# Performance work log

Hardware: AMD Instinct MI355X
Metric: run time of the kernel (lower is better)

Reference implementation:

```python
import jax, jax.numpy as jnp
import numpy as np

N = 4096  # rows == cols so the original's range(len(d1)) loop covers the full tensor
EPS = 1e-05


def setup_inputs() -> dict:
    key = jax.random.key(0)
    k1, k2 = jax.random.split(key)
    distribution1 = jax.random.uniform(k1, (N, N), dtype=jnp.float32)
    distribution2 = jax.random.uniform(k2, (N, N), dtype=jnp.float32)
    return {"distribution1": distribution1, "distribution2": distribution2}


def reference(distribution1, distribution2):
    d1 = jnp.squeeze(distribution1).astype(jnp.float32)
    d2 = jnp.squeeze(distribution2).astype(jnp.float32)
    # loss = sum_i [ -sum_j d1[i,j] * log(d2[i,j] + eps) ]  (fused elementwise + full reduce)
    loss = -jnp.sum(d1 * jnp.log(d2 + EPS))
    return loss.reshape(1)
```

## Files before the change

### kernel.cpp

```cpp
#include <hip/hip_runtime.h>
#include <math.h>


#define EPS 1e-5f
#define BLOCK 256
#define GRID 2048
#define STRIDE (GRID * BLOCK)

typedef float f4v __attribute__((ext_vector_type(4)));

#define LOAD2(Y, X, PB, PA)                                          \
    asm volatile("global_load_dwordx4 %0, %2, off sc0 sc1 nt\n\t"    \
                 "global_load_dwordx4 %1, %3, off sc0 sc1 nt"        \
                 : "=&v"(Y), "=&v"(X)                                \
                 : "v"(PB), "v"(PA)                                  \
                 : "memory")

#define WAITV(N)                                              \
    do {                                                      \
        asm volatile("s_waitcnt vmcnt(" #N ")" ::: "memory"); \
        __builtin_amdgcn_sched_barrier(0);                    \
    } while (0)

#define CP(X, Y)                                              \
    do {                                                      \
        acc0 = fmaf((X).x, __logf((Y).x + EPS), acc0);        \
        acc1 = fmaf((X).y, __logf((Y).y + EPS), acc1);        \
        acc2 = fmaf((X).z, __logf((Y).z + EPS), acc2);        \
        acc3 = fmaf((X).w, __logf((Y).w + EPS), acc3);        \
    } while (0)

__global__ __launch_bounds__(BLOCK) void cep_loss_kernel(
        const f4v* __restrict__ d1,
        const f4v* __restrict__ d2,
        float* __restrict__ partials) {
    const int tid = blockIdx.x * BLOCK + threadIdx.x;
    const f4v* pa = d1 + tid;
    const f4v* pb = d2 + tid;

    float acc0 = 0.0f, acc1 = 0.0f, acc2 = 0.0f, acc3 = 0.0f;

    f4v x0, x1, x2, x3, x4, x5, x6, x7;
    f4v y0, y1, y2, y3, y4, y5, y6, y7;

    LOAD2(y0, x0, pb, pa); pb += STRIDE; pa += STRIDE;
    LOAD2(y1, x1, pb, pa); pb += STRIDE; pa += STRIDE;
    LOAD2(y2, x2, pb, pa); pb += STRIDE; pa += STRIDE;
    LOAD2(y3, x3, pb, pa); pb += STRIDE; pa += STRIDE;

    WAITV(6); LOAD2(y4, x4, pb, pa); pb += STRIDE; pa += STRIDE; CP(x0, y0);
    WAITV(6); LOAD2(y5, x5, pb, pa); pb += STRIDE; pa += STRIDE; CP(x1, y1);
    WAITV(6); LOAD2(y6, x6, pb, pa); pb += STRIDE; pa += STRIDE; CP(x2, y2);
    WAITV(6); LOAD2(y7, x7, pb, pa);                             CP(x3, y3);

    WAITV(6); CP(x4, y4);
    WAITV(4); CP(x5, y5);
    WAITV(2); CP(x6, y6);
    WAITV(0); CP(x7, y7);

    float acc = (acc0 + acc1) + (acc2 + acc3);

    #pragma unroll
    for (int off = 32; off > 0; off >>= 1)
        acc += __shfl_down(acc, off, 64);

    __shared__ float wave_sums[BLOCK / 64];
    int lane = threadIdx.x & 63;
    int wid  = threadIdx.x >> 6;
    if (lane == 0) wave_sums[wid] = acc;
    __syncthreads();

    if (threadIdx.x == 0) {
        float s = wave_sums[0] + wave_sums[1] + wave_sums[2] + wave_sums[3];
        partials[blockIdx.x] = s;
    }
}

__global__ __launch_bounds__(BLOCK) void cep_final_kernel(
        const float* __restrict__ partials, float* __restrict__ out, int nparts) {
    float acc = 0.0f;
    for (int i = threadIdx.x; i < nparts; i += BLOCK)
        acc += partials[i];

    #pragma unroll
    for (int off = 32; off > 0; off >>= 1)
        acc += __shfl_down(acc, off, 64);

    __shared__ float wave_sums[BLOCK / 64];
    int lane = threadIdx.x & 63;
    int wid  = threadIdx.x >> 6;
    if (lane == 0) wave_sums[wid] = acc;
    __syncthreads();

    if (threadIdx.x == 0) {
        float s = wave_sums[0] + wave_sums[1] + wave_sums[2] + wave_sums[3];
        out[0] = -s;
    }
}

extern "C" void kernel_launch(void* const* d_in, const int* in_sizes, int n_in,
                              void* d_out, int out_size, void* d_ws, size_t ws_size,
                              hipStream_t stream) {
    const f4v* d1 = (const f4v*)d_in[0];
    const f4v* d2 = (const f4v*)d_in[1];
    float* out      = (float*)d_out;
    float* partials = (float*)d_ws;

    cep_loss_kernel<<<GRID, BLOCK, 0, stream>>>(d1, d2, partials);
    cep_final_kernel<<<1, BLOCK, 0, stream>>>(partials, out, GRID);
}
```

Baseline: 139.7 us.

## Route distribution2 loads through direct global-to-LDS async copies

```diff
diff --git a/kernel.cpp b/kernel.cpp
--- a/kernel.cpp
+++ b/kernel.cpp
@@ -9,17 +9,23 @@
 
 typedef float f4v __attribute__((ext_vector_type(4)));
 
-#define LOAD2(Y, X, PB, PA)                                          \
-    asm volatile("global_load_dwordx4 %0, %2, off sc0 sc1 nt\n\t"    \
-                 "global_load_dwordx4 %1, %3, off sc0 sc1 nt"        \
-                 : "=&v"(Y), "=&v"(X)                                \
-                 : "v"(PB), "v"(PA)                                  \
-                 : "memory")
+#define AS1 __attribute__((address_space(1)))
+#define AS3 __attribute__((address_space(3)))
+
+#define LOADX(X, PA)                                                 \
+    asm volatile("global_load_dwordx4 %0, %1, off sc0 sc1 nt"        \
+                 : "=&v"(X) : "v"(PA) : "memory")
 
 #define WAITV(N)                                              \
     do {                                                      \
         asm volatile("s_waitcnt vmcnt(" #N ")" ::: "memory"); \
         __builtin_amdgcn_sched_barrier(0);                    \
+    } while (0)
+
+#define WAITLGKM()                                              \
+    do {                                                        \
+        asm volatile("s_waitcnt lgkmcnt(0)" ::: "memory");      \
+        __builtin_amdgcn_sched_barrier(0);                      \
     } while (0)
 
 #define CP(X, Y)                                              \
@@ -34,29 +40,35 @@
         const f4v* __restrict__ d1,
         const f4v* __restrict__ d2,
         float* __restrict__ partials) {
+    __shared__ f4v sB[4][BLOCK];
+
     const int tid = blockIdx.x * BLOCK + threadIdx.x;
+    const int wb  = threadIdx.x & ~63;
     const f4v* pa = d1 + tid;
     const f4v* pb = d2 + tid;
 
     float acc0 = 0.0f, acc1 = 0.0f, acc2 = 0.0f, acc3 = 0.0f;
+    f4v x0, x1, x2, x3, x4, x5, x6, x7;
 
-    f4v x0, x1, x2, x3, x4, x5, x6, x7;
-    f4v y0, y1, y2, y3, y4, y5, y6, y7;
+#define ISSUE(BUF, X)                                                    \
+    do {                                                                 \
+        __builtin_amdgcn_global_load_lds(                                \
+            (const AS1 void*)pb, (AS3 void*)&sB[BUF][wb], 16, 0, 0);     \
+        LOADX(X, pa);                                                    \
+        pb += STRIDE; pa += STRIDE;                                      \
+    } while (0)
 
-    LOAD2(y0, x0, pb, pa); pb += STRIDE; pa += STRIDE;
-    LOAD2(y1, x1, pb, pa); pb += STRIDE; pa += STRIDE;
-    LOAD2(y2, x2, pb, pa); pb += STRIDE; pa += STRIDE;
-    LOAD2(y3, x3, pb, pa); pb += STRIDE; pa += STRIDE;
+    ISSUE(0, x0); ISSUE(1, x1); ISSUE(2, x2); ISSUE(3, x3);
 
-    WAITV(6); LOAD2(y4, x4, pb, pa); pb += STRIDE; pa += STRIDE; CP(x0, y0);
-    WAITV(6); LOAD2(y5, x5, pb, pa); pb += STRIDE; pa += STRIDE; CP(x1, y1);
-    WAITV(6); LOAD2(y6, x6, pb, pa); pb += STRIDE; pa += STRIDE; CP(x2, y2);
-    WAITV(6); LOAD2(y7, x7, pb, pa);                             CP(x3, y3);
-
-    WAITV(6); CP(x4, y4);
-    WAITV(4); CP(x5, y5);
-    WAITV(2); CP(x6, y6);
-    WAITV(0); CP(x7, y7);
+    f4v y;
+    WAITV(6); y = sB[0][threadIdx.x]; WAITLGKM(); ISSUE(0, x4); CP(x0, y);
+    WAITV(6); y = sB[1][threadIdx.x]; WAITLGKM(); ISSUE(1, x5); CP(x1, y);
+    WAITV(6); y = sB[2][threadIdx.x]; WAITLGKM(); ISSUE(2, x6); CP(x2, y);
+    WAITV(6); y = sB[3][threadIdx.x]; WAITLGKM(); ISSUE(3, x7); CP(x3, y);
+    WAITV(6); y = sB[0][threadIdx.x]; CP(x4, y);
+    WAITV(4); y = sB[1][threadIdx.x]; CP(x5, y);
+    WAITV(2); y = sB[2][threadIdx.x]; CP(x6, y);
+    WAITV(0); y = sB[3][threadIdx.x]; CP(x7, y);
 
     float acc = (acc0 + acc1) + (acc2 + acc3);
 
```

After: 133.0 us, median of 2. -4.8%, faster.
